# Kernel optimization log

Hardware: AMD Instinct MI355X
Metric: run time of the kernel (lower is better)

## Reference

```python
import jax, jax.numpy as jnp
import numpy as np

B, N, CIN, D, K, H, W = 1, 65536, 5, 128, 16, 64, 1024
EPS = 1e-5


def _bn(x, g, b, m, v, ch_axis):
    shape = [1] * x.ndim
    shape[ch_axis] = -1
    return (x - m.reshape(shape)) * jax.lax.rsqrt(v.reshape(shape) + EPS) * g.reshape(shape) + b.reshape(shape)


def setup_inputs() -> dict:
    key = jax.random.key(0)
    ks = jax.random.split(key, 10)
    s = 0.05
    return {
        "pc": jax.random.normal(ks[0], (B, N, CIN), jnp.float32),
        "neighbors": jax.random.randint(ks[1], (B, N, K), 0, N),
        "px": jax.random.randint(ks[2], (N,), 0, W),
        "py": jax.random.randint(ks[3], (N,), 0, H),
        "norm_gamma": jnp.ones((CIN,), jnp.float32),
        "norm_beta": jnp.zeros((CIN,), jnp.float32),
        "norm_mean": jnp.zeros((CIN,), jnp.float32),
        "norm_var": jnp.ones((CIN,), jnp.float32),
        "conv1_w": jax.random.normal(ks[4], (D, CIN), jnp.float32) * s,
        "conv1_b": jnp.zeros((D,), jnp.float32),
        "bn2a_gamma": jnp.ones((CIN,), jnp.float32),
        "bn2a_beta": jnp.zeros((CIN,), jnp.float32),
        "bn2a_mean": jnp.zeros((CIN,), jnp.float32),
        "bn2a_var": jnp.ones((CIN,), jnp.float32),
        "w2a": jax.random.normal(ks[5], (D, CIN), jnp.float32) * s,
        "bn2b_gamma": jnp.ones((D,), jnp.float32),
        "bn2b_beta": jnp.zeros((D,), jnp.float32),
        "bn2b_mean": jnp.zeros((D,), jnp.float32),
        "bn2b_var": jnp.ones((D,), jnp.float32),
        "w2b": jax.random.normal(ks[6], (D, D), jnp.float32) * s,
        "final_w": jax.random.normal(ks[7], (D, 2 * D), jnp.float32) * s,
        "final_b": jnp.zeros((D,), jnp.float32),
    }


def reference(pc, neighbors, px, py,
              norm_gamma, norm_beta, norm_mean, norm_var,
              conv1_w, conv1_b,
              bn2a_gamma, bn2a_beta, bn2a_mean, bn2a_var, w2a,
              bn2b_gamma, bn2b_beta, bn2b_mean, bn2b_var, w2b,
              final_w, final_b):
    # pc: [B, N, CIN] -> channels-first [B, CIN, N]
    x = jnp.transpose(pc, (0, 2, 1))
    x = _bn(x, norm_gamma, norm_beta, norm_mean, norm_var, 1)  # BatchNorm1d (eval)
    # point embedding: 1x1 conv1d
    point_emb = jnp.einsum('dc,bcn->bdn', conv1_w, x) + conv1_b[None, :, None]
    # neighbor gather (skip self at k=0): idx [B, K-1, N]
    nb = jnp.transpose(neighbors, (0, 2, 1))
    idx = nb[:, 1:, :]
    # gathered: [B, CIN, K-1, N]
    gathered = jnp.take_along_axis(x[:, :, None, :], idx[:, None, :, :], axis=3)
    neigh = gathered - x[:, :, None, :]  # per-neighbor difference
    # shared MLP: BN2d -> 1x1 conv (no bias) -> BN2d -> GELU -> 1x1 conv (no bias)
    h = _bn(neigh, bn2a_gamma, bn2a_beta, bn2a_mean, bn2a_var, 1)
    h = jnp.einsum('dc,bckn->bdkn', w2a, h)
    h = _bn(h, bn2b_gamma, bn2b_beta, bn2b_mean, bn2b_var, 1)
    h = jax.nn.gelu(h, approximate=False)  # torch nn.GELU default = exact erf
    h = jnp.einsum('ed,bdkn->bekn', w2b, h)
    neigh_emb = jnp.max(h, axis=2)  # max over neighbors -> [B, D, N]
    feats = jnp.einsum('df,bfn->bdn', final_w,
                       jnp.concatenate([point_emb, neigh_emb], axis=1)) + final_b[None, :, None]
    # scatter into range image (B assumed 1, as in original squeeze(0))
    proj = jnp.full((H, W, D), -1.0, dtype=jnp.float32)
    proj = proj.at[py, px].set(feats[0].T)
    return jnp.transpose(proj, (2, 0, 1))[None]  # [1, D, H, W]
```

## Files before the change

kernel.cpp:

```cpp
#include <hip/hip_runtime.h>

#define NPTS 65536
#define WW 1024
#define HWCELLS 65536
#define EPSF 1e-5f
#define QPTS 16

typedef __attribute__((ext_vector_type(8))) short short8;
typedef __attribute__((ext_vector_type(4))) float f32x4;

__device__ __forceinline__ float gelu_f(float x) {
    float x2 = x * x;
    float q  = fmaf(x2, -0.1029432f, -2.3022160f);
    float e  = __builtin_amdgcn_exp2f(x * q);
    float r  = __builtin_amdgcn_rcpf(1.0f + e);
    return x * r;
}
__device__ __forceinline__ unsigned f2bf_rne(float x) {
    unsigned u = __float_as_uint(x);
    return (u + 0x7fffu + ((u >> 16) & 1u)) >> 16;
}
__device__ __forceinline__ unsigned cvtpk(float lo, float hi) {
    unsigned r;
    asm("v_cvt_pk_bf16_f32 %0, %1, %2" : "=v"(r) : "v"(lo), "v"(hi));
    return r;
}

__global__ void prepfold_k(const float* __restrict__ pc, const int* __restrict__ px,
                           const int* __restrict__ py,
                           float4* __restrict__ xn4, float* __restrict__ xn1,
                           int* __restrict__ winner,
                           const float* __restrict__ ng, const float* __restrict__ nbta,
                           const float* __restrict__ nm, const float* __restrict__ nv,
                           const float* __restrict__ w2a,
                           const float* __restrict__ g2a, const float* __restrict__ b2a,
                           const float* __restrict__ m2a, const float* __restrict__ v2a,
                           const float* __restrict__ g2b, const float* __restrict__ b2b,
                           const float* __restrict__ m2b, const float* __restrict__ v2b,
                           const float* __restrict__ w2b,
                           const float* __restrict__ c1w, const float* __restrict__ c1b,
                           const float* __restrict__ fw, const float* __restrict__ fbias,
                           unsigned short* __restrict__ w2aB8,
                           unsigned short* __restrict__ w2bB,
                           unsigned short* __restrict__ fwallB) {
    __shared__ float c1wS[640];
    __shared__ float c1adjS[128];
    const int t = threadIdx.x;

    if (blockIdx.x < 256) {
        int i = blockIdx.x * 256 + t;
        const float* p = &pc[(size_t)i * 5];
        xn4[i] = make_float4(p[0], p[1], p[2], p[3]);
        xn1[i] = p[4];
        int cell = py[i] * WW + px[i];
        atomicMax(&winner[cell], i);
        return;
    }

    const int d = t;
    float s_n[5], t_n[5];
#pragma unroll
    for (int c = 0; c < 5; ++c) {
        s_n[c] = ng[c] * rsqrtf(nv[c] + EPSF);
        t_n[c] = nbta[c] - nm[c] * s_n[c];
    }
    for (int j = t; j < 640; j += 256) c1wS[j] = c1w[j];
    __syncthreads();
    if (t < 128) {
        float a = c1b[d];
#pragma unroll
        for (int c = 0; c < 5; ++c) a += c1wS[d * 5 + c] * t_n[c];
        c1adjS[d] = a;
    }
    __syncthreads();
    if (t >= 128) return;

    float s2b = g2b[d] * rsqrtf(v2b[d] + EPSF);
    float t2b = b2b[d] - m2b[d] * s2b;
    float acc = 0.f;
#pragma unroll
    for (int c = 0; c < 5; ++c) {
        float s2a = g2a[c] * rsqrtf(v2a[c] + EPSF);
        float t2a = b2a[c] - m2a[c] * s2a;
        float wv = w2a[d * 5 + c];
        w2aB8[d * 8 + c] = (unsigned short)f2bf_rne(s2b * wv * s2a * s_n[c]);
        acc += s2b * wv * t2a;
    }
    w2aB8[d * 8 + 5] = (unsigned short)f2bf_rne(acc + t2b);
    w2aB8[d * 8 + 6] = 0; w2aB8[d * 8 + 7] = 0;

#pragma unroll 8
    for (int i4 = 0; i4 < 32; ++i4) {
        float4 v = *(const float4*)&w2b[d * 128 + i4 * 4];
        unsigned short* dst = &w2bB[d * 128 + i4 * 4];
        dst[0] = (unsigned short)f2bf_rne(v.x);
        dst[1] = (unsigned short)f2bf_rne(v.y);
        dst[2] = (unsigned short)f2bf_rne(v.z);
        dst[3] = (unsigned short)f2bf_rne(v.w);
    }

    float f1[5] = {0.f, 0.f, 0.f, 0.f, 0.f};
    float fbv = fbias[d];
#pragma unroll 8
    for (int d4 = 0; d4 < 32; ++d4) {
        float4 fv = *(const float4*)&fw[d * 256 + d4 * 4];
        float4 fn = *(const float4*)&fw[d * 256 + 128 + d4 * 4];
        unsigned short* dst = &fwallB[d * 160 + d4 * 4];
        dst[0] = (unsigned short)f2bf_rne(fn.x);
        dst[1] = (unsigned short)f2bf_rne(fn.y);
        dst[2] = (unsigned short)f2bf_rne(fn.z);
        dst[3] = (unsigned short)f2bf_rne(fn.w);
        int dd = d4 * 4;
        fbv += fv.x * c1adjS[dd] + fv.y * c1adjS[dd+1] + fv.z * c1adjS[dd+2] + fv.w * c1adjS[dd+3];
#pragma unroll
        for (int c = 0; c < 5; ++c)
            f1[c] += fv.x * c1wS[dd*5 + c] + fv.y * c1wS[(dd+1)*5 + c]
                   + fv.z * c1wS[(dd+2)*5 + c] + fv.w * c1wS[(dd+3)*5 + c];
    }
#pragma unroll
    for (int c = 0; c < 5; ++c)
        fwallB[d * 160 + 128 + c] = (unsigned short)f2bf_rne(f1[c] * s_n[c]);
    fwallB[d * 160 + 133] = (unsigned short)f2bf_rne(fbv);
    for (int j = 134; j < 160; ++j) fwallB[d * 160 + j] = 0;
}

__global__ void cntout_k(float4* __restrict__ out4,
                         const int* __restrict__ winner, int* __restrict__ blockcnt) {
    int gid = blockIdx.x * 256 + threadIdx.x;
    float4 mone = make_float4(-1.f, -1.f, -1.f, -1.f);
#pragma unroll
    for (int j = 0; j < 8; ++j) out4[gid + j * 262144] = mone;
    if (blockIdx.x >= 256) return;
    bool occ = winner[gid] >= 0;
    unsigned long long m = __ballot(occ);
    __shared__ int wcnt[4];
    int lane = threadIdx.x & 63, wv = threadIdx.x >> 6;
    if (lane == 0) wcnt[wv] = __popcll(m);
    __syncthreads();
    if (threadIdx.x == 0)
        blockcnt[blockIdx.x] = wcnt[0] + wcnt[1] + wcnt[2] + wcnt[3];
}

__global__ void fillscan_k(const int* __restrict__ winner,
                           const int* __restrict__ blockcnt,
                           int* __restrict__ ids, int* __restrict__ cells,
                           int* __restrict__ count) {
    __shared__ int s[256];
    __shared__ int wcnt[4];
    int t = threadIdx.x;
    s[t] = blockcnt[t];
    __syncthreads();
    for (int off = 1; off < 256; off <<= 1) {
        int v = (t >= off) ? s[t - off] : 0;
        __syncthreads();
        s[t] += v;
        __syncthreads();
    }
    if (blockIdx.x == 0 && t == 255) *count = s[255];
    int excl = s[blockIdx.x] - blockcnt[blockIdx.x];

    int cell = blockIdx.x * 256 + t;
    int win = winner[cell];
    bool occ = win >= 0;
    unsigned long long m = __ballot(occ);
    int lane = t & 63, wv = t >> 6;
    if (lane == 0) wcnt[wv] = __popcll(m);
    __syncthreads();
    int woff = excl;
    for (int i = 0; i < wv; ++i) woff += wcnt[i];
    if (occ) {
        int lrank = __popcll(m & ((1ull << lane) - 1));
        ids[woff + lrank] = win;
        cells[woff + lrank] = cell;
    }
}

__launch_bounds__(256, 6)
__global__ void main_k(const int* __restrict__ ids, const int* __restrict__ cells,
                       const int* __restrict__ countp,
                       const int* __restrict__ nbrs,
                       const float4* __restrict__ xn4, const float* __restrict__ xn1,
                       const unsigned short* __restrict__ w2aB8,
                       const unsigned short* __restrict__ w2bB,
                       const unsigned short* __restrict__ fwallB,
                       float* __restrict__ outp) {
    const int cnt = *countp;
    const int n0 = blockIdx.x * QPTS;
    if (n0 >= cnt) return;

    __shared__ char           lds[8192];
    __shared__ unsigned short dxS[15 * 16 * 8];
    __shared__ int   idS[QPTS];
    __shared__ int   nbS[QPTS * 16];
    __shared__ float xnS[QPTS][5];
    __shared__ int   cellS[QPTS];

    const int t = threadIdx.x;
    const int w = t >> 6;
    const int l = t & 63;
    const int l15 = l & 15;
    const int lg  = l >> 4;

    if (t < QPTS) {
        int slot = n0 + t;
        slot = slot < cnt ? slot : cnt - 1;
        idS[t] = ids[slot];
        cellS[t] = cells[slot];
    }
    __syncthreads();

    nbS[t] = nbrs[idS[t >> 4] * 16 + (t & 15)];
    if (t < QPTS) {
        int id = idS[t];
        float4 a = xn4[id];
        xnS[t][0] = a.x; xnS[t][1] = a.y; xnS[t][2] = a.z; xnS[t][3] = a.w;
        xnS[t][4] = xn1[id];
    }

    short8 a1[2] = { {0,0,0,0,0,0,0,0}, {0,0,0,0,0,0,0,0} };
    if (lg == 0) {
        a1[0] = *(const short8*)(w2aB8 + (w * 32 + l15) * 8);
        a1[1] = *(const short8*)(w2aB8 + (w * 32 + 16 + l15) * 8);
    }
    short8 a2[2][4];
#pragma unroll
    for (int rt = 0; rt < 2; ++rt)
#pragma unroll
        for (int ks = 0; ks < 4; ++ks)
            a2[rt][ks] = *(const short8*)(w2bB + (w * 32 + rt * 16 + l15) * 128 + ks * 32 + lg * 8);

    __syncthreads();

    if (t < 240) {
        int pt = t & 15, kk = t >> 4;
        int nb = nbS[pt * 16 + kk + 1];
        float4 a = xn4[nb];
        float  e = xn1[nb];
        float d0 = a.x - xnS[pt][0];
        float d1 = a.y - xnS[pt][1];
        float d2 = a.z - xnS[pt][2];
        float d3 = a.w - xnS[pt][3];
        float d4 = e   - xnS[pt][4];
        uint4 v;
        v.x = cvtpk(d0, d1);
        v.y = cvtpk(d2, d3);
        v.z = cvtpk(d4, 1.0f);
        v.w = 0u;
        *(uint4*)&dxS[(kk * 16 + pt) * 8] = v;
    }
    __syncthreads();

    const f32x4 zero4 = {0.f, 0.f, 0.f, 0.f};
    f32x4 mmax[2];
#pragma unroll
    for (int rt = 0; rt < 2; ++rt)
#pragma unroll
        for (int j = 0; j < 4; ++j) mmax[rt][j] = -1e30f;

    for (int kk = 0; kk < 15; ++kk) {
        short8 dxf = *(const short8*)&dxS[(kk * 16 + l15) * 8];
        char* Gb = lds + (kk & 1) * 4096;
#pragma unroll
        for (int rt = 0; rt < 2; ++rt) {
            f32x4 s = __builtin_amdgcn_mfma_f32_16x16x32_bf16(a1[rt], dxf, zero4, 0, 0, 0);
            uint2 pr;
            pr.x = cvtpk(gelu_f(s[0]), gelu_f(s[1]));
            pr.y = cvtpk(gelu_f(s[2]), gelu_f(s[3]));
            int din0 = w * 32 + rt * 16 + lg * 4;
            *(uint2*)(Gb + l15 * 256 + ((din0 * 2) ^ (l15 << 4))) = pr;
        }
        __syncthreads();
        f32x4 acc[2];
        __builtin_amdgcn_s_setprio(1);
#pragma unroll
        for (int ks = 0; ks < 4; ++ks) {
            int kb = (ks * 32 + lg * 8) * 2;
            short8 bfrag = *(const short8*)(Gb + l15 * 256 + (kb ^ (l15 << 4)));
#pragma unroll
            for (int rt = 0; rt < 2; ++rt)
                acc[rt] = __builtin_amdgcn_mfma_f32_16x16x32_bf16(
                    a2[rt][ks], bfrag, ks == 0 ? zero4 : acc[rt], 0, 0, 0);
        }
        __builtin_amdgcn_s_setprio(0);
#pragma unroll
        for (int rt = 0; rt < 2; ++rt)
#pragma unroll
            for (int j = 0; j < 4; ++j)
                mmax[rt][j] = fmaxf(mmax[rt][j], acc[rt][j]);
    }

    __syncthreads();

    {
        char* Mb = lds;
        int sw = l15 << 4;
#pragma unroll
        for (int rt = 0; rt < 2; ++rt) {
            int dout = w * 32 + rt * 16 + lg * 4;
            unsigned lo = cvtpk(mmax[rt][0], mmax[rt][1]);
            unsigned hi = cvtpk(mmax[rt][2], mmax[rt][3]);
            *(unsigned*)(Mb + l15 * 320 + ((dout * 2) ^ sw)) = lo;
            *(unsigned*)(Mb + l15 * 320 + (((dout + 2) * 2) ^ sw)) = hi;
        }
        if (t < QPTS) {
            uint4 a;
            a.x = cvtpk(xnS[t][0], xnS[t][1]);
            a.y = cvtpk(xnS[t][2], xnS[t][3]);
            a.z = cvtpk(xnS[t][4], 1.0f);
            a.w = 0u;
            uint4 z; z.x = 0u; z.y = 0u; z.z = 0u; z.w = 0u;
            *(uint4*)(Mb + t * 320 + 256) = a;
            *(uint4*)(Mb + t * 320 + 272) = z;
            *(uint4*)(Mb + t * 320 + 288) = z;
            *(uint4*)(Mb + t * 320 + 304) = z;
        }
    }
    __syncthreads();

    f32x4 facc[2];
    const char* Mr = lds;
#pragma unroll
    for (int ks = 0; ks < 5; ++ks) {
        short8 af[2];
#pragma unroll
        for (int rt = 0; rt < 2; ++rt)
            af[rt] = *(const short8*)(fwallB + (w * 32 + rt * 16 + l15) * 160 + ks * 32 + lg * 8);
        int kb = (ks * 32 + lg * 8) * 2;
        int kbs = (kb < 256) ? (kb ^ (l15 << 4)) : kb;
        short8 bfr = *(const short8*)(Mr + l15 * 320 + kbs);
#pragma unroll
        for (int rt = 0; rt < 2; ++rt)
            facc[rt] = __builtin_amdgcn_mfma_f32_16x16x32_bf16(
                af[rt], bfr, ks == 0 ? zero4 : facc[rt], 0, 0, 0);
    }

    const int cell = cellS[l15];
#pragma unroll
    for (int rt = 0; rt < 2; ++rt) {
        int e0 = w * 32 + rt * 16 + lg * 4;
#pragma unroll
        for (int j = 0; j < 4; ++j)
            outp[(size_t)(e0 + j) * HWCELLS + cell] = facc[rt][j];
    }
}

extern "C" void kernel_launch(void* const* d_in, const int* in_sizes, int n_in,
                              void* d_out, int out_size, void* d_ws, size_t ws_size,
                              hipStream_t stream) {
    const float* pc        = (const float*)d_in[0];
    const int*   neighbors = (const int*)d_in[1];
    const int*   px        = (const int*)d_in[2];
    const int*   py        = (const int*)d_in[3];
    const float* norm_g    = (const float*)d_in[4];
    const float* norm_b    = (const float*)d_in[5];
    const float* norm_m    = (const float*)d_in[6];
    const float* norm_v    = (const float*)d_in[7];
    const float* conv1_w   = (const float*)d_in[8];
    const float* conv1_b   = (const float*)d_in[9];
    const float* bn2a_g    = (const float*)d_in[10];
    const float* bn2a_b    = (const float*)d_in[11];
    const float* bn2a_m    = (const float*)d_in[12];
    const float* bn2a_v    = (const float*)d_in[13];
    const float* w2a       = (const float*)d_in[14];
    const float* bn2b_g    = (const float*)d_in[15];
    const float* bn2b_b    = (const float*)d_in[16];
    const float* bn2b_m    = (const float*)d_in[17];
    const float* bn2b_v    = (const float*)d_in[18];
    const float* w2b       = (const float*)d_in[19];
    const float* final_w   = (const float*)d_in[20];
    const float* final_b   = (const float*)d_in[21];
    float* out = (float*)d_out;

    char* ws = (char*)d_ws;
    float4*         xn4      = (float4*)(ws);
    float*          xn1      = (float*)(ws + 1048576);
    int*            winner   = (int*)(ws + 1310720);
    int*            ids      = (int*)(ws + 1572864);
    int*            cells    = (int*)(ws + 1835008);
    int*            count    = (int*)(ws + 2097152);
    int*            blockcnt = (int*)(ws + 2097408);
    unsigned short* w2aB8    = (unsigned short*)(ws + 2098432);
    unsigned short* w2bB     = (unsigned short*)(ws + 2100480);
    unsigned short* fwallB   = (unsigned short*)(ws + 2133248);

    hipMemsetAsync(winner, 0xFF, 262144, stream);
    prepfold_k<<<257, 256, 0, stream>>>(pc, px, py, xn4, xn1, winner,
                                        norm_g, norm_b, norm_m, norm_v,
                                        w2a, bn2a_g, bn2a_b, bn2a_m, bn2a_v,
                                        bn2b_g, bn2b_b, bn2b_m, bn2b_v, w2b,
                                        conv1_w, conv1_b, final_w, final_b,
                                        w2aB8, w2bB, fwallB);
    cntout_k<<<1024, 256, 0, stream>>>((float4*)out, winner, blockcnt);
    fillscan_k<<<256, 256, 0, stream>>>(winner, blockcnt, ids, cells, count);
    main_k<<<4096, 256, 0, stream>>>(ids, cells, count, neighbors, xn4, xn1,
                                     w2aB8, w2bB, fwallB, out);
}
```

Before: 98.36 us.

## Fuse the -1 output fill into main kernel with coalesced staged row writes

The separate kernel pass that filled the whole output with -1 is removed; the counting kernel now only counts occupied cells. Each main_k block instead owns the span of cells from its first occupied cell up to the next block's first occupied cell. It stages its features in LDS, builds a cell-to-slot map, and writes full contiguous output rows, filling gaps with -1. This drops a full extra pass over the output and replaces scattered 4-byte stores with coalesced ones, at the cost of extra LDS traffic and barriers. The launch-bounds occupancy hint is also raised from 6 to 8 blocks per CU, which may add register pressure.

```diff
diff --git a/kernel.cpp b/kernel.cpp
--- a/kernel.cpp
+++ b/kernel.cpp
@@ -124,13 +124,8 @@
     for (int j = 134; j < 160; ++j) fwallB[d * 160 + j] = 0;
 }
 
-__global__ void cntout_k(float4* __restrict__ out4,
-                         const int* __restrict__ winner, int* __restrict__ blockcnt) {
+__global__ void cnt_k(const int* __restrict__ winner, int* __restrict__ blockcnt) {
     int gid = blockIdx.x * 256 + threadIdx.x;
-    float4 mone = make_float4(-1.f, -1.f, -1.f, -1.f);
-#pragma unroll
-    for (int j = 0; j < 8; ++j) out4[gid + j * 262144] = mone;
-    if (blockIdx.x >= 256) return;
     bool occ = winner[gid] >= 0;
     unsigned long long m = __ballot(occ);
     __shared__ int wcnt[4];
@@ -175,7 +170,7 @@
     }
 }
 
-__launch_bounds__(256, 6)
+__launch_bounds__(256, 8)
 __global__ void main_k(const int* __restrict__ ids, const int* __restrict__ cells,
                        const int* __restrict__ countp,
                        const int* __restrict__ nbrs,
@@ -188,7 +183,7 @@
     const int n0 = blockIdx.x * QPTS;
     if (n0 >= cnt) return;
 
-    __shared__ char           lds[8192];
+    __shared__ char           lds[8448];
     __shared__ unsigned short dxS[15 * 16 * 8];
     __shared__ int   idS[QPTS];
     __shared__ int   nbS[QPTS * 16];
@@ -334,13 +329,43 @@
                 af[rt], bfr, ks == 0 ? zero4 : facc[rt], 0, 0, 0);
     }
 
-    const int cell = cellS[l15];
+    __syncthreads();
+
+    float* featsF = (float*)lds;
 #pragma unroll
     for (int rt = 0; rt < 2; ++rt) {
         int e0 = w * 32 + rt * 16 + lg * 4;
 #pragma unroll
         for (int j = 0; j < 4; ++j)
-            outp[(size_t)(e0 + j) * HWCELLS + cell] = facc[rt][j];
+            featsF[l15 * 132 + e0 + j] = facc[rt][j];
+    }
+
+    int* slotmap = (int*)dxS;
+    const int cend = (n0 + QPTS >= cnt) ? HWCELLS : cells[n0 + QPTS];
+    const int c0 = (blockIdx.x == 0) ? 0 : cellS[0];
+    __syncthreads();
+
+    for (int chunk0 = c0; chunk0 < cend; chunk0 += 960) {
+        int L = cend - chunk0; L = L < 960 ? L : 960;
+        for (int i = t; i < L; i += 256) slotmap[i] = -1;
+        __syncthreads();
+        if (t < QPTS) {
+            int cc = cellS[t];
+            if (cc >= chunk0 && cc < chunk0 + L) slotmap[cc - chunk0] = t;
+        }
+        __syncthreads();
+        int ci0 = t & 31, eq = t >> 5;
+#pragma unroll 4
+        for (int ep = 0; ep < 16; ++ep) {
+            int e = ep * 8 + eq;
+            float* orow = outp + (size_t)e * HWCELLS + chunk0;
+            for (int cb = ci0; cb < L; cb += 32) {
+                int slot = slotmap[cb];
+                float v = (slot >= 0) ? featsF[slot * 132 + e] : -1.0f;
+                orow[cb] = v;
+            }
+        }
+        __syncthreads();
     }
 }
 
@@ -390,7 +415,7 @@
                                         bn2b_g, bn2b_b, bn2b_m, bn2b_v, w2b,
                                         conv1_w, conv1_b, final_w, final_b,
                                         w2aB8, w2bB, fwallB);
-    cntout_k<<<1024, 256, 0, stream>>>((float4*)out, winner, blockcnt);
+    cnt_k<<<256, 256, 0, stream>>>(winner, blockcnt);
     fillscan_k<<<256, 256, 0, stream>>>(winner, blockcnt, ids, cells, count);
     main_k<<<4096, 256, 0, stream>>>(ids, cells, count, neighbors, xn4, xn1,
                                      w2aB8, w2bB, fwallB, out);
```

After: 126.9 us. 1.29x slower.
